# Kernel optimization log

Measured on AMD Instinct MI355X. Metric: run time of the kernel, lower is better.

The kernel has to match this reference:

```python
import jax, jax.numpy as jnp
import numpy as np

V = 32000      # vocab size
D = 256        # embedding_dim
HOPS = 3       # max_hops
MAXS = 1024    # max_s (positional table has MAXS+1 rows)
PAD = 0        # pad_id


def _pos_table(n_position, d):
    pos = np.arange(n_position)[:, None].astype(np.float64)
    j = np.arange(d)[None, :]
    angle = pos / np.power(10000.0, 2 * (j // 2) / d)
    tab = angle.copy()
    tab[1:, 0::2] = np.sin(angle[1:, 0::2])
    tab[1:, 1::2] = np.cos(angle[1:, 1::2])
    tab[0] = 0.0
    return jnp.asarray(tab, dtype=jnp.float32)


def setup_inputs() -> dict:
    key = jax.random.key(0)
    ks = jax.random.split(key, 10)
    M, B, T = 1024, 32, 4
    story = jax.random.randint(ks[0], (M, B, T), 0, V, dtype=jnp.int64)
    enc_query = jax.random.randint(ks[1], (B,), 0, V, dtype=jnp.int64)
    last_hidden = jax.random.normal(ks[2], (1, B, D), dtype=jnp.float32)
    # C_0..C_HOPS embedding tables, N(0, 0.1), pad row zeroed (padding_idx)
    C = 0.1 * jax.random.normal(ks[3], (HOPS + 1, V, D), dtype=jnp.float32)
    C = C.at[:, PAD].set(0.0)
    pos_table = _pos_table(MAXS + 1, D)
    W1_w = 0.02 * jax.random.normal(ks[4], (V, 2 * D), dtype=jnp.float32)
    W1_b = jnp.zeros((V,), dtype=jnp.float32)
    gru_w_ih = 0.05 * jax.random.normal(ks[5], (3 * D, D), dtype=jnp.float32)
    gru_w_hh = 0.05 * jax.random.normal(ks[6], (3 * D, D), dtype=jnp.float32)
    gru_b_ih = 0.05 * jax.random.normal(ks[7], (3 * D,), dtype=jnp.float32)
    gru_b_hh = 0.05 * jax.random.normal(ks[8], (3 * D,), dtype=jnp.float32)
    return {"story": story, "enc_query": enc_query, "last_hidden": last_hidden,
            "C": C, "pos_table": pos_table, "W1_w": W1_w, "W1_b": W1_b,
            "gru_w_ih": gru_w_ih, "gru_w_hh": gru_w_hh,
            "gru_b_ih": gru_b_ih, "gru_b_hh": gru_b_hh}


def _gru_step(x, h, w_ih, w_hh, b_ih, b_hh):
    # single-step torch.nn.GRU cell math; x,h: [B, D]
    gi = x @ w_ih.T + b_ih
    gh = h @ w_hh.T + b_hh
    i_r, i_z, i_n = jnp.split(gi, 3, axis=-1)
    h_r, h_z, h_n = jnp.split(gh, 3, axis=-1)
    r = jax.nn.sigmoid(i_r + h_r)
    z = jax.nn.sigmoid(i_z + h_z)
    n = jnp.tanh(i_n + r * h_n)
    return (1.0 - z) * n + z * h


def reference(story, enc_query, last_hidden, C, pos_table, W1_w, W1_b,
              gru_w_ih, gru_w_hh, gru_b_ih, gru_b_hh):
    # --- load_memory ---
    s = jnp.transpose(story, (1, 0, 2))            # [B, M, T]
    pad_mask = s[:, :, 0] == PAD                   # [B, M]
    positions = jnp.cumsum((~pad_mask).astype(jnp.int32), axis=-1)
    positions = jnp.where(pad_mask, 0, positions)
    embed_pos = pos_table[positions]               # [B, M, D]
    m_story = []
    for hop in range(HOPS + 1):
        m_A = C[hop][s].sum(axis=2)                # gather [B,M,T,D] -> sum over T
        if hop == 0:
            m_A = m_A + embed_pos
        m_story.append(m_A)
    # --- ptrMemDecoder ---
    embed_q = C[0][enc_query]                      # [B, D]
    h_new = _gru_step(embed_q, last_hidden[0], gru_w_ih, gru_w_hh, gru_b_ih, gru_b_hh)
    hidden = h_new[None]                           # [1, B, D]
    u = h_new
    u0 = h_new
    p_vocab = None
    prob_lg = None
    for hop in range(HOPS):
        m_A = m_story[hop]
        prob_lg = jnp.einsum('bmd,bd->bm', m_A, u)
        prob = jax.nn.softmax(prob_lg, axis=1)
        m_C = m_story[hop + 1]
        o_k = jnp.einsum('bm,bmd->bd', prob, m_C)
        if hop == 0:
            p_vocab = jnp.concatenate([u0, o_k], axis=1) @ W1_w.T + W1_b
        u = u + o_k
    return prob_lg, p_vocab, hidden
```

## Files before the change

### kernel.cpp

```cpp
#include <hip/hip_runtime.h>
#include <hip/hip_bf16.h>

#define VSZ 32000
#define DSZ 256
#define BSZ 32
#define MSZ 1024
#define PSZ 1025
#define VD  (VSZ * DSZ)
#define XBP 264

#define OFF_U     32768
#define OFF_U0    40960
#define OFF_PP    49152
#define OFF_GIH   81952
#define OFF_SC    131104
#define OFF_PMAX  163872
#define OFF_PSUM  167968
#define OFF_PROJ  172064

#define OUT_PV  (BSZ * MSZ)
#define OUT_HID (OUT_PV + BSZ * VSZ)

typedef __attribute__((ext_vector_type(8))) short bfrag;
typedef __attribute__((ext_vector_type(4))) float f32x4;

__device__ __forceinline__ short bfc(float f) {
    __hip_bfloat16 h = __float2bfloat16(f);
    return __builtin_bit_cast(short, h);
}

__device__ __forceinline__ bfrag cvt8(float4 a, float4 b) {
    bfrag f;
    f[0] = bfc(a.x); f[1] = bfc(a.y); f[2] = bfc(a.z); f[3] = bfc(a.w);
    f[4] = bfc(b.x); f[5] = bfc(b.y); f[6] = bfc(b.z); f[7] = bfc(b.w);
    return f;
}

__device__ __forceinline__ void stage_xb(const float* __restrict__ src,
                                         short* __restrict__ xB, int t) {
    for (int i = t; i < BSZ * 64; i += 256) {
        int b = i >> 6, c4 = i & 63;
        float4 v = ((const float4*)src)[i];
        short4 pk = make_short4(bfc(v.x), bfc(v.y), bfc(v.z), bfc(v.w));
        *(short4*)&xB[(size_t)b * XBP + c4 * 4] = pk;
    }
}

__device__ __forceinline__ void stage_xb_diff(const float* __restrict__ a,
                                              const float* __restrict__ c,
                                              short* __restrict__ xB, int t) {
    for (int i = t; i < BSZ * 64; i += 256) {
        int b = i >> 6, c4 = i & 63;
        float4 va = ((const float4*)a)[i];
        float4 vc = ((const float4*)c)[i];
        short4 pk = make_short4(bfc(va.x - vc.x), bfc(va.y - vc.y),
                                bfc(va.z - vc.z), bfc(va.w - vc.w));
        *(short4*)&xB[(size_t)b * XBP + c4 * 4] = pk;
    }
}

template <int NRT>
__device__ __forceinline__ void mfma_deep(
    const float* __restrict__ W, int wstride, int rbeg, int nrows,
    const short* __restrict__ xB, f32x4 (&acc)[NRT][2], int t)
{
    const int lane = t & 63, w = t >> 6;
    const int m = lane & 15, kg = lane >> 4;
    bfrag xb[8][2];
#pragma unroll
    for (int kc = 0; kc < 8; ++kc) {
        xb[kc][0] = *(const bfrag*)&xB[(size_t)m * XBP + kc * 32 + kg * 8];
        xb[kc][1] = *(const bfrag*)&xB[(size_t)(16 + m) * XBP + kc * 32 + kg * 8];
    }
    const float* wp[NRT];
#pragma unroll
    for (int rt = 0; rt < NRT; ++rt) {
        int r = w * (NRT * 16) + rt * 16 + m;
        int rc = (r < nrows) ? r : 0;
        wp[rt] = W + (size_t)(rbeg + rc) * wstride + kg * 8;
    }
    float4 wbuf[4][NRT][2];
#pragma unroll
    for (int p = 0; p < 4; ++p)
#pragma unroll
        for (int rt = 0; rt < NRT; ++rt) {
            wbuf[p][rt][0] = *(const float4*)(wp[rt] + p * 32);
            wbuf[p][rt][1] = *(const float4*)(wp[rt] + p * 32 + 4);
        }
#pragma unroll
    for (int kt = 0; kt < 8; ++kt) {
        const int s = kt & 3;
#pragma unroll
        for (int rt = 0; rt < NRT; ++rt) {
            bfrag af = cvt8(wbuf[s][rt][0], wbuf[s][rt][1]);
            acc[rt][0] = __builtin_amdgcn_mfma_f32_16x16x32_bf16(af, xb[kt][0], acc[rt][0], 0, 0, 0);
            acc[rt][1] = __builtin_amdgcn_mfma_f32_16x16x32_bf16(af, xb[kt][1], acc[rt][1], 0, 0, 0);
        }
        if (kt < 4) {
#pragma unroll
            for (int rt = 0; rt < NRT; ++rt) {
                wbuf[s][rt][0] = *(const float4*)(wp[rt] + (kt + 4) * 32);
                wbuf[s][rt][1] = *(const float4*)(wp[rt] + (kt + 4) * 32 + 4);
            }
        }
    }
}

template <int NRT>
__device__ __forceinline__ void mfma_store(
    const f32x4 (&acc)[NRT][2], float* __restrict__ dest,
    const float* __restrict__ bias, size_t drow, size_t dcol,
    int rbeg, int nrows, int t)
{
    const int lane = t & 63, w = t >> 6;
    const int n = lane & 15, rq = lane >> 4;
#pragma unroll
    for (int rt = 0; rt < NRT; ++rt) {
#pragma unroll
        for (int g = 0; g < 4; ++g) {
            int r = w * (NRT * 16) + rt * 16 + rq * 4 + g;
            if (r < nrows) {
                float bv = bias ? bias[rbeg + r] : 0.f;
                dest[(size_t)(rbeg + r) * drow + (size_t)n * dcol] = acc[rt][0][g] + bv;
                dest[(size_t)(rbeg + r) * drow + (size_t)(16 + n) * dcol] = acc[rt][1][g] + bv;
            }
        }
    }
}

template <int NRT>
__device__ __forceinline__ void acc_zero(f32x4 (&acc)[NRT][2]) {
#pragma unroll
    for (int rt = 0; rt < NRT; ++rt)
#pragma unroll
        for (int bt = 0; bt < 2; ++bt) {
            f32x4 z = {0.f, 0.f, 0.f, 0.f};
            acc[rt][bt] = z;
        }
}

__global__ __launch_bounds__(256, 1) void k_posgru(
    const int* __restrict__ story, const int* __restrict__ encq,
    const float* __restrict__ lasth, const float* __restrict__ C0,
    const float* __restrict__ gwih, const float* __restrict__ gwhh,
    int* __restrict__ pos, float* __restrict__ gih)
{
    __shared__ short xB[32 * XBP];
    __shared__ int wtot[4];
    int gid = blockIdx.x, t = threadIdx.x;
    int lane = t & 63, wid = t >> 6;
    if (gid < 32) {
        int b = gid, m0 = t * 4;
        int f0 = story[(size_t)((m0 + 0) * BSZ + b) * 4] != 0;
        int f1 = story[(size_t)((m0 + 1) * BSZ + b) * 4] != 0;
        int f2 = story[(size_t)((m0 + 2) * BSZ + b) * 4] != 0;
        int f3 = story[(size_t)((m0 + 3) * BSZ + b) * 4] != 0;
        int p1 = f0 + f1, p2 = p1 + f2, p3 = p2 + f3;
        int x = p3;
        for (int o = 1; o < 64; o <<= 1) {
            int v = __shfl_up(x, o, 64);
            if (lane >= o) x += v;
        }
        if (lane == 63) wtot[wid] = x;
        __syncthreads();
        int wo = 0;
        for (int i = 0; i < wid; ++i) wo += wtot[i];
        int base = wo + x - p3;
        pos[(m0 + 0) * BSZ + b] = f0 ? base + f0 : 0;
        pos[(m0 + 1) * BSZ + b] = f1 ? base + p1 : 0;
        pos[(m0 + 2) * BSZ + b] = f2 ? base + p2 : 0;
        pos[(m0 + 3) * BSZ + b] = f3 ? base + p3 : 0;
    } else {
        int k = gid - 32;
        bool isX = (k < 6);
        for (int i = t; i < BSZ * 64; i += 256) {
            int b = i >> 6, c4 = i & 63;
            float4 v = isX ? ((const float4*)(C0 + (size_t)encq[b] * DSZ))[c4]
                           : ((const float4*)(lasth + (size_t)b * DSZ))[c4];
            short4 pk = make_short4(bfc(v.x), bfc(v.y), bfc(v.z), bfc(v.w));
            *(short4*)&xB[(size_t)b * XBP + c4 * 4] = pk;
        }
        __syncthreads();
        int kr = isX ? k : k - 6;
        const float* W = isX ? gwih : gwhh;
        float* dest = gih + (isX ? 0 : 768 * BSZ);
        f32x4 acc[2][2];
        acc_zero<2>(acc);
        mfma_deep<2>(W, DSZ, kr * 128, 128, xB, acc, t);
        mfma_store<2>(acc, dest, nullptr, BSZ, 1, kr * 128, 128, t);
    }
}

__global__ void k_grufin(const float* __restrict__ gih,
                         const float* __restrict__ gbih, const float* __restrict__ gbhh,
                         const float* __restrict__ lasth,
                         float* __restrict__ u, float* __restrict__ u0,
                         float* __restrict__ hid)
{
    int idx = blockIdx.x * 256 + threadIdx.x;
    int b = idx & 31, d = idx >> 5;
    float gi0 = gih[(size_t)(0 * DSZ + d) * BSZ + b] + gbih[0 * DSZ + d];
    float gi1 = gih[(size_t)(1 * DSZ + d) * BSZ + b] + gbih[1 * DSZ + d];
    float gi2 = gih[(size_t)(2 * DSZ + d) * BSZ + b] + gbih[2 * DSZ + d];
    float gh0 = gih[(size_t)(3 * DSZ + d) * BSZ + b] + gbhh[0 * DSZ + d];
    float gh1 = gih[(size_t)(4 * DSZ + d) * BSZ + b] + gbhh[1 * DSZ + d];
    float gh2 = gih[(size_t)(5 * DSZ + d) * BSZ + b] + gbhh[2 * DSZ + d];
    float r = 1.f / (1.f + __expf(-(gi0 + gh0)));
    float z = 1.f / (1.f + __expf(-(gi1 + gh1)));
    float n = tanhf(gi2 + r * gh2);
    float h = lasth[(size_t)b * DSZ + d];
    float hn = (1.f - z) * n + z * h;
    int o = b * DSZ + d;
    u[o] = hn; u0[o] = hn; hid[o] = hn;
}

__global__ __launch_bounds__(256, 1) void k_proj(
    const float* __restrict__ Ct, const float* __restrict__ postab,
    const float* __restrict__ u, float* __restrict__ proj,
    float* __restrict__ pp, int nproj)
{
    __shared__ short xB[32 * XBP];
    int gid = blockIdx.x, t = threadIdx.x;
    stage_xb(u, xB, t);
    __syncthreads();
    f32x4 acc[2][2];
    acc_zero<2>(acc);
    if (gid < nproj) {
        int rb = gid * 128;
        mfma_deep<2>(Ct, DSZ, rb, 128, xB, acc, t);
        mfma_store<2>(acc, proj, nullptr, 1, VSZ, rb, 128, t);
    } else {
        int rb = (gid - nproj) * 128;
        int nr = min(128, PSZ - rb);
        mfma_deep<2>(postab, DSZ, rb, nr, xB, acc, t);
        mfma_store<2>(acc, pp, nullptr, 1, PSZ, rb, nr, t);
    }
}

__global__ void k_scores(const int* __restrict__ story, const int* __restrict__ pos,
                         const float* __restrict__ proj, const float* __restrict__ pp,
                         float* __restrict__ sc, float* __restrict__ pmax,
                         float* __restrict__ psum, float* __restrict__ outlg, int hop)
{
    __shared__ float red[256];
    int gid = blockIdx.x, t = threadIdx.x;
    int idx = gid * 256 + t;
    int b = idx & 31, m = idx >> 5;
    int4 st = *(const int4*)&story[(size_t)idx * 4];
    const float* pb = proj + (size_t)b * VSZ;
    float s = pb[st.x] + pb[st.y] + pb[st.z] + pb[st.w];
    if (hop == 0) s += pp[(size_t)b * PSZ + pos[idx]];
    if (hop == 2) { outlg[b * MSZ + m] = s; return; }
    sc[idx] = s;
    red[t] = s;
    __syncthreads();
    if (t < 32) {
        float mx = red[t];
#pragma unroll
        for (int k = 1; k < 8; ++k) mx = fmaxf(mx, red[k * 32 + t]);
        float sm = 0.f;
#pragma unroll
        for (int k = 0; k < 8; ++k) sm += __expf(red[k * 32 + t] - mx);
        pmax[gid * 32 + t] = mx;
        psum[gid * 32 + t] = sm;
    }
}

__global__ __launch_bounds__(256) void k_okpv(
    const int* __restrict__ story, const float* __restrict__ sc,
    const float* __restrict__ pmax, const float* __restrict__ psum,
    const float* __restrict__ Ct, float* __restrict__ u)
{
    int b = blockIdx.x & 31, mc = blockIdx.x >> 5;
    int t = threadIdx.x;
    __shared__ float red[256];
    __shared__ float pl[32];
    __shared__ float4 pt[4][64];
    red[t] = (t < 128) ? pmax[t * 32 + b] : -3.4e38f;
    __syncthreads();
    for (int o = 128; o >= 1; o >>= 1) {
        if (t < o) red[t] = fmaxf(red[t], red[t + o]);
        __syncthreads();
    }
    float M = red[0];
    __syncthreads();
    red[t] = (t < 128) ? psum[t * 32 + b] * __expf(pmax[t * 32 + b] - M) : 0.f;
    __syncthreads();
    for (int o = 128; o >= 1; o >>= 1) {
        if (t < o) red[t] += red[t + o];
        __syncthreads();
    }
    float S = red[0];
    __syncthreads();
    if (t < 32) pl[t] = __expf(sc[(size_t)(mc * 32 + t) * BSZ + b] - M) / S;
    __syncthreads();
    int dl = t & 63, mg = t >> 6;
    int mbase = mc * 32 + mg * 8;
    float4 acc = make_float4(0.f, 0.f, 0.f, 0.f);
    int4 st = *(const int4*)&story[(size_t)(mbase * BSZ + b) * 4];
    float pw = pl[mg * 8];
#pragma unroll
    for (int i = 0; i < 8; ++i) {
        int4 s_ = st; float p_ = pw;
        if (i < 7) {
            st = *(const int4*)&story[(size_t)((mbase + i + 1) * BSZ + b) * 4];
            pw = pl[mg * 8 + i + 1];
        }
        float4 a0 = ((const float4*)(Ct + (size_t)s_.x * DSZ))[dl];
        float4 a1 = ((const float4*)(Ct + (size_t)s_.y * DSZ))[dl];
        float4 a2 = ((const float4*)(Ct + (size_t)s_.z * DSZ))[dl];
        float4 a3 = ((const float4*)(Ct + (size_t)s_.w * DSZ))[dl];
        acc.x += p_ * (a0.x + a1.x + a2.x + a3.x);
        acc.y += p_ * (a0.y + a1.y + a2.y + a3.y);
        acc.z += p_ * (a0.z + a1.z + a2.z + a3.z);
        acc.w += p_ * (a0.w + a1.w + a2.w + a3.w);
    }
    pt[mg][dl] = acc;
    __syncthreads();
    if (t < 64) {
        float4 s0 = pt[0][t], s1 = pt[1][t], s2 = pt[2][t], s3 = pt[3][t];
        float* dst = &u[(size_t)b * DSZ + t * 4];
        atomicAdd(dst + 0, s0.x + s1.x + s2.x + s3.x);
        atomicAdd(dst + 1, s0.y + s1.y + s2.y + s3.y);
        atomicAdd(dst + 2, s0.z + s1.z + s2.z + s3.z);
        atomicAdd(dst + 3, s0.w + s1.w + s2.w + s3.w);
    }
}

__global__ __launch_bounds__(256, 1) void k_tail0(
    const float* __restrict__ C1, const float* __restrict__ u,
    const float* __restrict__ u0, const float* __restrict__ W1w,
    const float* __restrict__ W1b, float* __restrict__ proj,
    float* __restrict__ out_pv)
{
    __shared__ short xB[32 * XBP];
    int gid = blockIdx.x, t = threadIdx.x;
    f32x4 acc[2][2];
    acc_zero<2>(acc);
    if (gid < 250) {
        int rb = gid * 128;
        stage_xb(u0, xB, t);
        __syncthreads();
        mfma_deep<2>(W1w, 512, rb, 128, xB, acc, t);
        __syncthreads();
        stage_xb_diff(u, u0, xB, t);
        __syncthreads();
        mfma_deep<2>(W1w + 256, 512, rb, 128, xB, acc, t);
        mfma_store<2>(acc, out_pv, W1b, 1, VSZ, rb, 128, t);
    } else {
        stage_xb(u, xB, t);
        __syncthreads();
        int rb = (gid - 250) * 128;
        mfma_deep<2>(C1, DSZ, rb, 128, xB, acc, t);
        mfma_store<2>(acc, proj, nullptr, 1, VSZ, rb, 128, t);
    }
}

extern "C" void kernel_launch(void* const* d_in, const int* in_sizes, int n_in,
                              void* d_out, int out_size, void* d_ws, size_t ws_size,
                              hipStream_t stream) {
    const int*   story  = (const int*)d_in[0];
    const int*   encq   = (const int*)d_in[1];
    const float* lasth  = (const float*)d_in[2];
    const float* C      = (const float*)d_in[3];
    const float* postab = (const float*)d_in[4];
    const float* W1w    = (const float*)d_in[5];
    const float* W1b    = (const float*)d_in[6];
    const float* gwih   = (const float*)d_in[7];
    const float* gwhh   = (const float*)d_in[8];
    const float* gbih   = (const float*)d_in[9];
    const float* gbhh   = (const float*)d_in[10];

    float* out = (float*)d_out;
    float* wsf = (float*)d_ws;
    int*   pos  = (int*)d_ws;
    float* u    = wsf + OFF_U;
    float* u0   = wsf + OFF_U0;
    float* pp   = wsf + OFF_PP;
    float* gih  = wsf + OFF_GIH;
    float* sc   = wsf + OFF_SC;
    float* pmax = wsf + OFF_PMAX;
    float* psum = wsf + OFF_PSUM;
    float* proj = wsf + OFF_PROJ;

    k_posgru<<<44, 256, 0, stream>>>(story, encq, lasth, C, gwih, gwhh, pos, gih);
    k_grufin<<<32, 256, 0, stream>>>(gih, gbih, gbhh, lasth, u, u0, out + OUT_HID);
    k_proj<<<259, 256, 0, stream>>>(C, postab, u, proj, pp, 250);

    for (int hop = 0; hop < 3; ++hop) {
        k_scores<<<128, 256, 0, stream>>>(story, pos, proj, pp, sc, pmax, psum,
                                          out, hop);
        if (hop == 2) break;
        k_okpv<<<1024, 256, 0, stream>>>(story, sc, pmax, psum,
                                         C + (size_t)(hop + 1) * VD, u);
        if (hop == 0) {
            k_tail0<<<500, 256, 0, stream>>>(C + (size_t)VD, u, u0, W1w, W1b,
                                             proj, out + OUT_PV);
        } else {
            k_proj<<<250, 256, 0, stream>>>(C + (size_t)2 * VD, nullptr, u, proj,
                                            nullptr, 250);
        }
    }
}
```

Measured before the change: 121.6 us.

## Transpose projection layout to vocab-major and double-buffer gathers in okpv

The projection and positional-projection buffers are now stored vocab-major ([V][B]) instead of batch-major, so the 32 batch lanes that gather the same story token in k_scores read adjacent addresses rather than rows 128KB apart. In k_okpv all story indices and weights are loaded up front, and the embedding row gathers are double-buffered two steps ahead to keep more loads in flight. This raises register use, and the stores in mfma_store become strided differently, which may cost some write coalescing.

```diff
diff --git a/kernel.cpp b/kernel.cpp
--- a/kernel.cpp
+++ b/kernel.cpp
@@ -228,12 +228,12 @@
     if (gid < nproj) {
         int rb = gid * 128;
         mfma_deep<2>(Ct, DSZ, rb, 128, xB, acc, t);
-        mfma_store<2>(acc, proj, nullptr, 1, VSZ, rb, 128, t);
+        mfma_store<2>(acc, proj, nullptr, BSZ, 1, rb, 128, t);
     } else {
         int rb = (gid - nproj) * 128;
         int nr = min(128, PSZ - rb);
         mfma_deep<2>(postab, DSZ, rb, nr, xB, acc, t);
-        mfma_store<2>(acc, pp, nullptr, 1, PSZ, rb, nr, t);
+        mfma_store<2>(acc, pp, nullptr, BSZ, 1, rb, nr, t);
     }
 }
 
@@ -247,9 +247,9 @@
     int idx = gid * 256 + t;
     int b = idx & 31, m = idx >> 5;
     int4 st = *(const int4*)&story[(size_t)idx * 4];
-    const float* pb = proj + (size_t)b * VSZ;
-    float s = pb[st.x] + pb[st.y] + pb[st.z] + pb[st.w];
-    if (hop == 0) s += pp[(size_t)b * PSZ + pos[idx]];
+    float s = proj[(size_t)st.x * BSZ + b] + proj[(size_t)st.y * BSZ + b] +
+              proj[(size_t)st.z * BSZ + b] + proj[(size_t)st.w * BSZ + b];
+    if (hop == 0) s += pp[(size_t)pos[idx] * BSZ + b];
     if (hop == 2) { outlg[b * MSZ + m] = s; return; }
     sc[idx] = s;
     red[t] = s;
@@ -296,25 +296,35 @@
     __syncthreads();
     int dl = t & 63, mg = t >> 6;
     int mbase = mc * 32 + mg * 8;
+    int4 sts[8]; float pws[8];
+#pragma unroll
+    for (int i = 0; i < 8; ++i) {
+        sts[i] = *(const int4*)&story[(size_t)((mbase + i) * BSZ + b) * 4];
+        pws[i] = pl[mg * 8 + i];
+    }
     float4 acc = make_float4(0.f, 0.f, 0.f, 0.f);
-    int4 st = *(const int4*)&story[(size_t)(mbase * BSZ + b) * 4];
-    float pw = pl[mg * 8];
-#pragma unroll
-    for (int i = 0; i < 8; ++i) {
-        int4 s_ = st; float p_ = pw;
-        if (i < 7) {
-            st = *(const int4*)&story[(size_t)((mbase + i + 1) * BSZ + b) * 4];
-            pw = pl[mg * 8 + i + 1];
-        }
-        float4 a0 = ((const float4*)(Ct + (size_t)s_.x * DSZ))[dl];
-        float4 a1 = ((const float4*)(Ct + (size_t)s_.y * DSZ))[dl];
-        float4 a2 = ((const float4*)(Ct + (size_t)s_.z * DSZ))[dl];
-        float4 a3 = ((const float4*)(Ct + (size_t)s_.w * DSZ))[dl];
-        acc.x += p_ * (a0.x + a1.x + a2.x + a3.x);
-        acc.y += p_ * (a0.y + a1.y + a2.y + a3.y);
-        acc.z += p_ * (a0.z + a1.z + a2.z + a3.z);
-        acc.w += p_ * (a0.w + a1.w + a2.w + a3.w);
-    }
+    float4 bufA[4], bufB[4];
+#define LOADR(dst, s_)                                                \
+    dst[0] = ((const float4*)(Ct + (size_t)(s_).x * DSZ))[dl];        \
+    dst[1] = ((const float4*)(Ct + (size_t)(s_).y * DSZ))[dl];        \
+    dst[2] = ((const float4*)(Ct + (size_t)(s_).z * DSZ))[dl];        \
+    dst[3] = ((const float4*)(Ct + (size_t)(s_).w * DSZ))[dl];
+#define STEP(i, CUR)                                                  \
+    {                                                                 \
+        float p_ = pws[i];                                            \
+        float4 a0 = CUR[0], a1 = CUR[1], a2 = CUR[2], a3 = CUR[3];    \
+        if ((i) + 2 < 8) { LOADR(CUR, sts[(i) + 2]); }                \
+        acc.x += p_ * (a0.x + a1.x + a2.x + a3.x);                    \
+        acc.y += p_ * (a0.y + a1.y + a2.y + a3.y);                    \
+        acc.z += p_ * (a0.z + a1.z + a2.z + a3.z);                    \
+        acc.w += p_ * (a0.w + a1.w + a2.w + a3.w);                    \
+    }
+    LOADR(bufA, sts[0]);
+    LOADR(bufB, sts[1]);
+    STEP(0, bufA) STEP(1, bufB) STEP(2, bufA) STEP(3, bufB)
+    STEP(4, bufA) STEP(5, bufB) STEP(6, bufA) STEP(7, bufB)
+#undef STEP
+#undef LOADR
     pt[mg][dl] = acc;
     __syncthreads();
     if (t < 64) {
@@ -352,7 +362,7 @@
         __syncthreads();
         int rb = (gid - 250) * 128;
         mfma_deep<2>(C1, DSZ, rb, 128, xB, acc, t);
-        mfma_store<2>(acc, proj, nullptr, 1, VSZ, rb, 128, t);
+        mfma_store<2>(acc, proj, nullptr, BSZ, 1, rb, 128, t);
     }
 }
 
```

Result: no change. 119.6 us (-1.6%).
